# Performance work log

Measured on AMD Instinct MI355X. Metric: run time of the kernel, lower is better.

## Reference

```python
import jax, jax.numpy as jnp
import numpy as np

B, L, D = 2, 2048, 2048
H, KV, HD = 16, 8, 128
EPS = 1e-5
ROPE_BASE = 10000.0
SCALING_ALPHA = 1.0
SCALE = HD ** -0.5


def setup_inputs() -> dict:
    key = jax.random.key(0)
    ks = jax.random.split(key, 5)
    s = 0.02  # weight init scale
    return {
        "x": jax.random.normal(ks[0], (B, L, D), jnp.float32),
        "wq": jax.random.normal(ks[1], (D, H * HD), jnp.float32) * s,
        "wk": jax.random.normal(ks[2], (D, KV * HD), jnp.float32) * s,
        "wv": jax.random.normal(ks[3], (D, KV * HD), jnp.float32) * s,
        "wo": jax.random.normal(ks[4], (H * HD, D), jnp.float32) * s,
        "qn_w": jnp.ones((HD,), jnp.float32),
        "kn_w": jnp.ones((HD,), jnp.float32),
    }


def _rope(t):
    # t: [B, h, L, HD]. DynamicNTKAlpha base scaling (alpha=1 -> no-op).
    base = ROPE_BASE * SCALING_ALPHA ** (HD / (HD - 2))
    # NOTE: source uses base**(+i/d) (no negative exponent) -- kept faithful.
    freqs = base ** (jnp.arange(0, HD, 2, dtype=jnp.float32) / HD)  # [HD/2]
    pos = jnp.arange(t.shape[-2], dtype=jnp.float32)                # [L]
    angles = pos[:, None] * freqs[None, :]                          # [L, HD/2]
    cos, sin = jnp.cos(angles), jnp.sin(angles)
    x1, x2 = t[..., : HD // 2], t[..., HD // 2 :]
    return jnp.concatenate([x1 * cos - x2 * sin, x2 * cos + x1 * sin], axis=-1)


def _rmsnorm(t, w):
    return t * jax.lax.rsqrt(jnp.mean(t * t, axis=-1, keepdims=True) + EPS) * w


def reference(x, wq, wk, wv, wo, qn_w, kn_w):
    b, l, _ = x.shape
    q = (x @ wq).reshape(b, l, H, HD).transpose(0, 2, 1, 3)   # [B,H,L,HD]
    k = (x @ wk).reshape(b, l, KV, HD).transpose(0, 2, 1, 3)  # [B,KV,L,HD]
    v = (x @ wv).reshape(b, l, KV, HD).transpose(0, 2, 1, 3)
    q = _rmsnorm(_rope(q), qn_w)
    k = _rmsnorm(_rope(k), kn_w)
    # GQA: expand KV heads to match query heads
    rep = H // KV
    k = jnp.repeat(k, rep, axis=1)  # [B,H,L,HD]
    v = jnp.repeat(v, rep, axis=1)
    scores = jnp.einsum("bhqd,bhkd->bhqk", q, k) * SCALE
    probs = jax.nn.softmax(scores, axis=-1)
    out = jnp.einsum("bhqk,bhkd->bhqd", probs, v)             # [B,H,L,HD]
    out = out.transpose(0, 2, 1, 3).reshape(b, l, H * HD)
    return out @ wo
```

## Files before the change

kernel.cpp:

```cpp
#include <hip/hip_runtime.h>
#include <math.h>

#define BB 2
#define LL 2048
#define DD 2048
#define HH 16
#define KVH 8
#define HDIM 128
#define SCALE_F 0.08838834764831845f
#define EPS_F 1e-5f
#define LOG2E 1.4426950408889634f
#define SMAX_F 17.0f
#define QKVW 4096

typedef unsigned short u16;
typedef __attribute__((ext_vector_type(8))) short short8;
typedef __attribute__((ext_vector_type(4))) float f32x4;
typedef __attribute__((ext_vector_type(16))) float f32x16;

#define MFMA16(a, b, c) __builtin_amdgcn_mfma_f32_16x16x32_bf16((a), (b), (c), 0, 0, 0)
#define MFMA32(a, b, c) __builtin_amdgcn_mfma_f32_32x32x16_bf16((a), (b), (c), 0, 0, 0)

__device__ __forceinline__ float b2f(u16 u) {
    union { unsigned int i; float f; } x;
    x.i = ((unsigned int)u) << 16;
    return x.f;
}
__device__ __forceinline__ u16 f2b(float f) {
    unsigned int x = __float_as_uint(f);
    unsigned int r = x + 0x7FFFu + ((x >> 16) & 1u);
    return (u16)(r >> 16);
}
__device__ __forceinline__ u16 f2b_fast(float f) {
    return (u16)((__float_as_uint(f) + 0x8000u) >> 16);
}
__device__ __forceinline__ void g2l(const u16* g, u16* l) {
    __builtin_amdgcn_global_load_lds(
        (const __attribute__((address_space(1))) unsigned int*)g,
        (__attribute__((address_space(3))) unsigned int*)l, 16, 0, 0);
}

__global__ __launch_bounds__(256) void convert_f32_bf16(const float* __restrict__ in,
                                                        u16* __restrict__ out, int n) {
    int i = (blockIdx.x * 256 + threadIdx.x) * 4;
    if (i >= n) return;
    float4 v = *(const float4*)(in + i);
    unsigned int p0 = (unsigned int)f2b(v.x) | ((unsigned int)f2b(v.y) << 16);
    unsigned int p1 = (unsigned int)f2b(v.z) | ((unsigned int)f2b(v.w) << 16);
    uint2 pk; pk.x = p0; pk.y = p1;
    *(uint2*)(out + i) = pk;
}

__global__ __launch_bounds__(256) void transpose_conv(const float* __restrict__ in,
                                                      u16* __restrict__ out, int R, int C) {
    __shared__ u16 t[64 * 65];
    int c0 = blockIdx.x * 64, r0 = blockIdx.y * 64;
#pragma unroll
    for (int i = 0; i < 16; i++) {
        int idx = threadIdx.x + i * 256;
        int r = idx >> 6, c = idx & 63;
        t[r * 65 + c] = f2b(in[(size_t)(r0 + r) * C + c0 + c]);
    }
    __syncthreads();
#pragma unroll
    for (int i = 0; i < 16; i++) {
        int idx = threadIdx.x + i * 256;
        int r = idx >> 6, c = idx & 63;
        out[(size_t)(c0 + r) * R + r0 + c] = t[c * 65 + r];
    }
}

__global__ __launch_bounds__(256) void transpose_v(const u16* __restrict__ qkv,
                                                   u16* __restrict__ vt) {
    __shared__ u16 t[64 * 65];
    int l0 = blockIdx.x * 64, d0 = blockIdx.y * 64;
    int bg = blockIdx.z, b = bg >> 3, g = bg & 7;
    const u16* src = qkv + (size_t)b * LL * QKVW + 3072 + g * HDIM;
    u16* dst = vt + (size_t)bg * HDIM * LL;
#pragma unroll
    for (int i = 0; i < 16; i++) {
        int idx = threadIdx.x + i * 256;
        int r = idx >> 6, c = idx & 63;
        t[r * 65 + c] = src[(size_t)(l0 + r) * QKVW + d0 + c];
    }
    __syncthreads();
#pragma unroll
    for (int i = 0; i < 16; i++) {
        int idx = threadIdx.x + i * 256;
        int r = idx >> 6, c = idx & 63;
        dst[(size_t)(d0 + r) * LL + l0 + c] = t[c * 65 + r];
    }
}

__global__ __launch_bounds__(256) void rope_table(float* __restrict__ ct, float* __restrict__ st) {
    int i = blockIdx.x * 256 + threadIdx.x;
    int pos = i >> 6, d = i & 63;
    float freq = (float)pow(10000.0, (double)d * (1.0 / 64.0));
    float ang = (float)pos * freq;
    double a = (double)ang;
    ct[i] = (float)cos(a);
    st[i] = (float)sin(a);
}

template <bool F32OUT>
__global__ __launch_bounds__(256) void gemm_bt(const u16* __restrict__ A,
                                               const u16* __restrict__ Bt,
                                               void* __restrict__ Cv, int M, int N, int K) {
    __shared__ __align__(16) u16 As[128 * 32];
    __shared__ __align__(16) u16 Bs[128 * 32];
    const int tid = threadIdx.x;
    const int w = tid >> 6, lane = tid & 63;
    const int lm = lane & 15, lq = lane >> 4;
    const int bn0 = blockIdx.x * 128, bm0 = blockIdx.y * 128;
    const int wm = (w >> 1) * 64, wn = (w & 1) * 64;

    f32x4 acc[4][4];
#pragma unroll
    for (int i = 0; i < 4; i++)
#pragma unroll
        for (int j = 0; j < 4; j++) acc[i][j] = (f32x4){0.f, 0.f, 0.f, 0.f};

    const int sr = w * 32 + (lane >> 2);
    const int scc = lane & 3;
    const u16* ga = A + (size_t)(bm0 + sr) * K + scc * 8;
    const u16* gb = Bt + (size_t)(bn0 + sr) * K + scc * 8;
    u16* lA = &As[w * 1024];
    u16* lB = &Bs[w * 1024];

    for (int k0 = 0; k0 < K; k0 += 32) {
        __syncthreads();
        g2l(ga + k0, lA);
        g2l(ga + (size_t)16 * K + k0, lA + 512);
        g2l(gb + k0, lB);
        g2l(gb + (size_t)16 * K + k0, lB + 512);
        __syncthreads();

        short8 af[4], bf[4];
#pragma unroll
        for (int mt = 0; mt < 4; mt++)
            af[mt] = *(const short8*)(&As[(wm + mt * 16 + lm) * 32 + lq * 8]);
#pragma unroll
        for (int nt = 0; nt < 4; nt++)
            bf[nt] = *(const short8*)(&Bs[(wn + nt * 16 + lm) * 32 + lq * 8]);
#pragma unroll
        for (int mt = 0; mt < 4; mt++)
#pragma unroll
            for (int nt = 0; nt < 4; nt++) acc[mt][nt] = MFMA16(af[mt], bf[nt], acc[mt][nt]);
    }

#pragma unroll
    for (int mt = 0; mt < 4; mt++)
#pragma unroll
        for (int nt = 0; nt < 4; nt++)
#pragma unroll
            for (int r = 0; r < 4; r++) {
                int row = bm0 + wm + mt * 16 + lq * 4 + r;
                int col = bn0 + wn + nt * 16 + lm;
                if (F32OUT)
                    ((float*)Cv)[(size_t)row * N + col] = acc[mt][nt][r];
                else
                    ((u16*)Cv)[(size_t)row * N + col] = f2b(acc[mt][nt][r]);
            }
}

__global__ __launch_bounds__(256) void rope_norm(u16* __restrict__ qkv,
                                                 const float* __restrict__ qw,
                                                 const float* __restrict__ kw,
                                                 const float* __restrict__ ct,
                                                 const float* __restrict__ st) {
    int slot = blockIdx.x * 4 + (threadIdx.x >> 6);
    int lane = threadIdx.x & 63;
    int hh = slot % (HH + KVH);
    int row = slot / (HH + KVH);
    int pos = row & (LL - 1);

    u16* base = qkv + (size_t)row * QKVW + hh * HDIM;
    const float* w = (hh < HH) ? qw : kw;

    float x1 = b2f(base[lane]), x2 = b2f(base[lane + 64]);
    float c = ct[pos * 64 + lane], s = st[pos * 64 + lane];
    float r1 = x1 * c - x2 * s;
    float r2 = x2 * c + x1 * s;
    float ss = r1 * r1 + r2 * r2;
#pragma unroll
    for (int m = 1; m < 64; m <<= 1) ss += __shfl_xor(ss, m, 64);
    float sc = 1.0f / sqrtf(ss * (1.0f / 128.0f) + EPS_F);
    base[lane] = f2b(r1 * sc * w[lane]);
    base[lane + 64] = f2b(r2 * sc * w[lane + 64]);
}

__global__ __launch_bounds__(256, 2) void attn_kernel(const u16* __restrict__ qkv,
                                                      const u16* __restrict__ vt,
                                                      u16* __restrict__ ob) {
    __shared__ __align__(16) u16 Kt[64 * 128];
    __shared__ __align__(16) u16 Vt[128 * 64];
    __shared__ __align__(16) u16 Ps[4][32 * 64];

    const int tid = threadIdx.x, w = tid >> 6, lane = tid & 63;
    const int l31 = lane & 31, lh = lane >> 5;
    const int q0 = blockIdx.x * 128;
    const int bh = blockIdx.y, b = bh >> 4, hd = bh & 15, g = hd >> 1;

    const u16* kbase = qkv + (size_t)b * LL * QKVW + 2048 + g * HDIM;
    const u16* vtbase = vt + (size_t)(b * KVH + g) * HDIM * LL;

    const int krl = lane >> 4, kgl = lane & 15;
    const int vrl = lane >> 3, vgl = lane & 7;

    const int qrow = q0 + w * 32 + l31;
    short8 aq[8];
    {
        const u16* qp = qkv + (size_t)(b * LL + qrow) * QKVW + hd * HDIM + lh * 8;
#pragma unroll
        for (int kk = 0; kk < 8; kk++) aq[kk] = *(const short8*)(qp + kk * 16);
    }

    f32x16 o[4];
#pragma unroll
    for (int i = 0; i < 4; i++)
#pragma unroll
        for (int r = 0; r < 16; r++) o[i][r] = 0.f;
    float psum[16];
#pragma unroll
    for (int r = 0; r < 16; r++) psum[r] = 0.f;
    const float SC2 = SCALE_F * LOG2E;

    for (int t = 0; t < LL / 64; t++) {
        __syncthreads();
#pragma unroll
        for (int ch = 0; ch < 4; ch++) {
            int r = w * 16 + ch * 4 + krl;
            int gc = kgl ^ (r & 15);
            g2l(kbase + (size_t)(t * 64 + r) * QKVW + gc * 8,
                &Kt[(w * 16 + ch * 4) * 128]);
        }
#pragma unroll
        for (int ch = 0; ch < 4; ch++) {
            int r = w * 32 + ch * 8 + vrl;
            int gc = vgl ^ (r & 7);
            g2l(vtbase + (size_t)r * LL + t * 64 + gc * 8,
                &Vt[(w * 32 + ch * 8) * 64]);
        }
        __syncthreads();

        f32x16 s[2];
#pragma unroll
        for (int kt = 0; kt < 2; kt++) {
#pragma unroll
            for (int r = 0; r < 16; r++) s[kt][r] = 0.f;
            int key = kt * 32 + l31;
#pragma unroll
            for (int kk = 0; kk < 8; kk++) {
                int gg = (kk * 2 + lh) ^ (key & 15);
                short8 bf = *(const short8*)(&Kt[key * 128 + gg * 8]);
                s[kt] = MFMA32(aq[kk], bf, s[kt]);
            }
        }

#pragma unroll
        for (int kt = 0; kt < 2; kt++) {
            int key = kt * 32 + l31;
#pragma unroll
            for (int r = 0; r < 16; r++) {
                float p = exp2f(fmaf(s[kt][r], SC2, -SMAX_F));
                psum[r] += p;
                int row = (r & 3) + 8 * (r >> 2) + 4 * lh;
                Ps[w][row * 64 + (key ^ ((row & 7) << 3))] = f2b_fast(p);
            }
        }
        __syncthreads();

#pragma unroll
        for (int kc = 0; kc < 4; kc++) {
            int gp = ((kc * 2 + lh) ^ (l31 & 7)) * 8;
            short8 pa = *(const short8*)(&Ps[w][l31 * 64 + gp]);
#pragma unroll
            for (int dn = 0; dn < 4; dn++) {
                int d = dn * 32 + l31;
                int gv = ((kc * 2 + lh) ^ (d & 7)) * 8;
                short8 bv = *(const short8*)(&Vt[d * 64 + gv]);
                o[dn] = MFMA32(pa, bv, o[dn]);
            }
        }
    }

#pragma unroll
    for (int m = 1; m < 32; m <<= 1)
#pragma unroll
        for (int r = 0; r < 16; r++) psum[r] += __shfl_xor(psum[r], m, 32);
    float inv[16];
#pragma unroll
    for (int r = 0; r < 16; r++) inv[r] = 1.0f / psum[r];

    u16* obase = ob + (size_t)(b * LL + q0 + w * 32) * (HH * HDIM) + hd * HDIM;
#pragma unroll
    for (int dn = 0; dn < 4; dn++)
#pragma unroll
        for (int r = 0; r < 16; r++) {
            int row = (r & 3) + 8 * (r >> 2) + 4 * lh;
            obase[(size_t)row * (HH * HDIM) + dn * 32 + l31] = f2b(o[dn][r] * inv[r]);
        }
}

extern "C" void kernel_launch(void* const* d_in, const int* in_sizes, int n_in,
                              void* d_out, int out_size, void* d_ws, size_t ws_size,
                              hipStream_t stream) {
    const float* x  = (const float*)d_in[0];
    const float* wq = (const float*)d_in[1];
    const float* wk = (const float*)d_in[2];
    const float* wv = (const float*)d_in[3];
    const float* wo = (const float*)d_in[4];
    const float* qn = (const float*)d_in[5];
    const float* kn = (const float*)d_in[6];

    u16* ws = (u16*)d_ws;
    const size_t SZ_X = (size_t)BB * LL * DD;
    u16* xb    = ws;
    u16* qkv   = xb + SZ_X;
    u16* wqkvT = qkv + (size_t)BB * LL * QKVW;
    u16* woT   = wqkvT + (size_t)QKVW * DD;
    float* ct  = (float*)(woT + (size_t)DD * DD);
    float* st  = ct + (size_t)LL * 64;
    u16* att = xb;
    u16* vt  = wqkvT;

    convert_f32_bf16<<<dim3((unsigned)(SZ_X / 1024)), dim3(256), 0, stream>>>(x, xb, (int)SZ_X);
    transpose_conv<<<dim3(32, 32), dim3(256), 0, stream>>>(wq, wqkvT, DD, DD);
    transpose_conv<<<dim3(16, 32), dim3(256), 0, stream>>>(wk, wqkvT + (size_t)2048 * DD, DD, KVH * HDIM);
    transpose_conv<<<dim3(16, 32), dim3(256), 0, stream>>>(wv, wqkvT + (size_t)3072 * DD, DD, KVH * HDIM);
    transpose_conv<<<dim3(32, 32), dim3(256), 0, stream>>>(wo, woT, HH * HDIM, DD);
    rope_table<<<dim3(LL * 64 / 256), dim3(256), 0, stream>>>(ct, st);

    gemm_bt<false><<<dim3(QKVW / 128, BB * LL / 128), dim3(256), 0, stream>>>(xb, wqkvT, qkv, BB * LL, QKVW, DD);

    rope_norm<<<dim3(BB * LL * (HH + KVH) / 4), dim3(256), 0, stream>>>(qkv, qn, kn, ct, st);
    transpose_v<<<dim3(LL / 64, HDIM / 64, BB * KVH), dim3(256), 0, stream>>>(qkv, vt);

    attn_kernel<<<dim3(LL / 128, BB * HH), dim3(256), 0, stream>>>(qkv, vt, att);
    gemm_bt<true><<<dim3(DD / 128, BB * LL / 128), dim3(256), 0, stream>>>(att, woT, d_out, BB * LL, DD, DD);
}
```

Measured before the change: 412.2 us.

## Merge prep and rope/V-transpose launches and split-K the output projection

The input conversion, the four weight transposes and the rope table build now run in one kernel that dispatches work by block-index range. Rope+RMSNorm and the V transpose are likewise combined into one launch, which cuts launch count and inter-kernel gaps. The output projection GEMM is split along K into two halves that accumulate into a zeroed fp32 output with atomicAdd, doubling the block count for better CU fill. The trade-off is an extra memset plus atomic write traffic on the output, and fp32 summation order that is no longer fixed.

```diff
diff --git a/kernel.cpp b/kernel.cpp
--- a/kernel.cpp
+++ b/kernel.cpp
@@ -40,72 +40,60 @@
         (__attribute__((address_space(3))) unsigned int*)l, 16, 0, 0);
 }
 
-__global__ __launch_bounds__(256) void convert_f32_bf16(const float* __restrict__ in,
-                                                        u16* __restrict__ out, int n) {
-    int i = (blockIdx.x * 256 + threadIdx.x) * 4;
-    if (i >= n) return;
-    float4 v = *(const float4*)(in + i);
-    unsigned int p0 = (unsigned int)f2b(v.x) | ((unsigned int)f2b(v.y) << 16);
-    unsigned int p1 = (unsigned int)f2b(v.z) | ((unsigned int)f2b(v.w) << 16);
-    uint2 pk; pk.x = p0; pk.y = p1;
-    *(uint2*)(out + i) = pk;
-}
-
-__global__ __launch_bounds__(256) void transpose_conv(const float* __restrict__ in,
-                                                      u16* __restrict__ out, int R, int C) {
+__global__ __launch_bounds__(256) void prep_kernel(const float* __restrict__ x,
+                                                   u16* __restrict__ xb,
+                                                   const float* __restrict__ wq,
+                                                   const float* __restrict__ wk,
+                                                   const float* __restrict__ wv,
+                                                   const float* __restrict__ wo,
+                                                   u16* __restrict__ wqkvT,
+                                                   u16* __restrict__ woT,
+                                                   float* __restrict__ ct,
+                                                   float* __restrict__ st) {
     __shared__ u16 t[64 * 65];
-    int c0 = blockIdx.x * 64, r0 = blockIdx.y * 64;
-#pragma unroll
-    for (int i = 0; i < 16; i++) {
-        int idx = threadIdx.x + i * 256;
-        int r = idx >> 6, c = idx & 63;
-        t[r * 65 + c] = f2b(in[(size_t)(r0 + r) * C + c0 + c]);
-    }
-    __syncthreads();
-#pragma unroll
-    for (int i = 0; i < 16; i++) {
-        int idx = threadIdx.x + i * 256;
-        int r = idx >> 6, c = idx & 63;
-        out[(size_t)(c0 + r) * R + r0 + c] = t[c * 65 + r];
-    }
-}
-
-__global__ __launch_bounds__(256) void transpose_v(const u16* __restrict__ qkv,
-                                                   u16* __restrict__ vt) {
-    __shared__ u16 t[64 * 65];
-    int l0 = blockIdx.x * 64, d0 = blockIdx.y * 64;
-    int bg = blockIdx.z, b = bg >> 3, g = bg & 7;
-    const u16* src = qkv + (size_t)b * LL * QKVW + 3072 + g * HDIM;
-    u16* dst = vt + (size_t)bg * HDIM * LL;
-#pragma unroll
-    for (int i = 0; i < 16; i++) {
-        int idx = threadIdx.x + i * 256;
-        int r = idx >> 6, c = idx & 63;
-        t[r * 65 + c] = src[(size_t)(l0 + r) * QKVW + d0 + c];
-    }
-    __syncthreads();
-#pragma unroll
-    for (int i = 0; i < 16; i++) {
-        int idx = threadIdx.x + i * 256;
-        int r = idx >> 6, c = idx & 63;
-        dst[(size_t)(d0 + r) * LL + l0 + c] = t[c * 65 + r];
-    }
-}
-
-__global__ __launch_bounds__(256) void rope_table(float* __restrict__ ct, float* __restrict__ st) {
-    int i = blockIdx.x * 256 + threadIdx.x;
-    int pos = i >> 6, d = i & 63;
-    float freq = (float)pow(10000.0, (double)d * (1.0 / 64.0));
-    float ang = (float)pos * freq;
-    double a = (double)ang;
-    ct[i] = (float)cos(a);
-    st[i] = (float)sin(a);
-}
-
-template <bool F32OUT>
+    const int blk = blockIdx.x, tid = threadIdx.x;
+    if (blk < 8192) {
+        int i = (blk * 256 + tid) * 4;
+        float4 v = *(const float4*)(x + i);
+        unsigned int p0 = (unsigned int)f2b(v.x) | ((unsigned int)f2b(v.y) << 16);
+        unsigned int p1 = (unsigned int)f2b(v.z) | ((unsigned int)f2b(v.w) << 16);
+        uint2 pk; pk.x = p0; pk.y = p1;
+        *(uint2*)(xb + i) = pk;
+    } else if (blk < 11264) {
+        int j = blk - 8192;
+        const float* in; u16* out; int C, bx, by;
+        if (j < 1024)      { in = wq; out = wqkvT;                      C = 2048; bx = j & 31; by = j >> 5; }
+        else if (j < 1536) { j -= 1024; in = wk; out = wqkvT + (size_t)2048 * DD; C = 1024; bx = j & 15; by = j >> 4; }
+        else if (j < 2048) { j -= 1536; in = wv; out = wqkvT + (size_t)3072 * DD; C = 1024; bx = j & 15; by = j >> 4; }
+        else               { j -= 2048; in = wo; out = woT;                      C = 2048; bx = j & 31; by = j >> 5; }
+        int c0 = bx * 64, r0 = by * 64;
+#pragma unroll
+        for (int i = 0; i < 16; i++) {
+            int idx = tid + i * 256;
+            int r = idx >> 6, c = idx & 63;
+            t[r * 65 + c] = f2b(in[(size_t)(r0 + r) * C + c0 + c]);
+        }
+        __syncthreads();
+#pragma unroll
+        for (int i = 0; i < 16; i++) {
+            int idx = tid + i * 256;
+            int r = idx >> 6, c = idx & 63;
+            out[(size_t)(c0 + r) * DD + r0 + c] = t[c * 65 + r];
+        }
+    } else {
+        int i = (blk - 11264) * 256 + tid;
+        int pos = i >> 6, d = i & 63;
+        float freq = (float)pow(10000.0, (double)d * (1.0 / 64.0));
+        float ang = (float)pos * freq;
+        double a = (double)ang;
+        ct[i] = (float)cos(a);
+        st[i] = (float)sin(a);
+    }
+}
+
 __global__ __launch_bounds__(256) void gemm_bt(const u16* __restrict__ A,
                                                const u16* __restrict__ Bt,
-                                               void* __restrict__ Cv, int M, int N, int K) {
+                                               u16* __restrict__ C, int M, int N, int K) {
     __shared__ __align__(16) u16 As[128 * 32];
     __shared__ __align__(16) u16 Bs[128 * 32];
     const int tid = threadIdx.x;
@@ -156,37 +144,117 @@
             for (int r = 0; r < 4; r++) {
                 int row = bm0 + wm + mt * 16 + lq * 4 + r;
                 int col = bn0 + wn + nt * 16 + lm;
-                if (F32OUT)
-                    ((float*)Cv)[(size_t)row * N + col] = acc[mt][nt][r];
-                else
-                    ((u16*)Cv)[(size_t)row * N + col] = f2b(acc[mt][nt][r]);
+                C[(size_t)row * N + col] = f2b(acc[mt][nt][r]);
             }
 }
 
-__global__ __launch_bounds__(256) void rope_norm(u16* __restrict__ qkv,
-                                                 const float* __restrict__ qw,
-                                                 const float* __restrict__ kw,
-                                                 const float* __restrict__ ct,
-                                                 const float* __restrict__ st) {
-    int slot = blockIdx.x * 4 + (threadIdx.x >> 6);
-    int lane = threadIdx.x & 63;
-    int hh = slot % (HH + KVH);
-    int row = slot / (HH + KVH);
-    int pos = row & (LL - 1);
-
-    u16* base = qkv + (size_t)row * QKVW + hh * HDIM;
-    const float* w = (hh < HH) ? qw : kw;
-
-    float x1 = b2f(base[lane]), x2 = b2f(base[lane + 64]);
-    float c = ct[pos * 64 + lane], s = st[pos * 64 + lane];
-    float r1 = x1 * c - x2 * s;
-    float r2 = x2 * c + x1 * s;
-    float ss = r1 * r1 + r2 * r2;
-#pragma unroll
-    for (int m = 1; m < 64; m <<= 1) ss += __shfl_xor(ss, m, 64);
-    float sc = 1.0f / sqrtf(ss * (1.0f / 128.0f) + EPS_F);
-    base[lane] = f2b(r1 * sc * w[lane]);
-    base[lane + 64] = f2b(r2 * sc * w[lane + 64]);
+__global__ __launch_bounds__(256) void gemm_bt_sk(const u16* __restrict__ A,
+                                                  const u16* __restrict__ Bt,
+                                                  float* __restrict__ C, int M, int N, int K) {
+    __shared__ __align__(16) u16 As[128 * 32];
+    __shared__ __align__(16) u16 Bs[128 * 32];
+    const int tid = threadIdx.x;
+    const int w = tid >> 6, lane = tid & 63;
+    const int lm = lane & 15, lq = lane >> 4;
+    const int bn0 = blockIdx.x * 128, bm0 = blockIdx.y * 128;
+    const int wm = (w >> 1) * 64, wn = (w & 1) * 64;
+    const int kbeg = blockIdx.z * (K >> 1), kend = kbeg + (K >> 1);
+
+    f32x4 acc[4][4];
+#pragma unroll
+    for (int i = 0; i < 4; i++)
+#pragma unroll
+        for (int j = 0; j < 4; j++) acc[i][j] = (f32x4){0.f, 0.f, 0.f, 0.f};
+
+    const int sr = w * 32 + (lane >> 2);
+    const int scc = lane & 3;
+    const u16* ga = A + (size_t)(bm0 + sr) * K + scc * 8;
+    const u16* gb = Bt + (size_t)(bn0 + sr) * K + scc * 8;
+    u16* lA = &As[w * 1024];
+    u16* lB = &Bs[w * 1024];
+
+    for (int k0 = kbeg; k0 < kend; k0 += 32) {
+        __syncthreads();
+        g2l(ga + k0, lA);
+        g2l(ga + (size_t)16 * K + k0, lA + 512);
+        g2l(gb + k0, lB);
+        g2l(gb + (size_t)16 * K + k0, lB + 512);
+        __syncthreads();
+
+        short8 af[4], bf[4];
+#pragma unroll
+        for (int mt = 0; mt < 4; mt++)
+            af[mt] = *(const short8*)(&As[(wm + mt * 16 + lm) * 32 + lq * 8]);
+#pragma unroll
+        for (int nt = 0; nt < 4; nt++)
+            bf[nt] = *(const short8*)(&Bs[(wn + nt * 16 + lm) * 32 + lq * 8]);
+#pragma unroll
+        for (int mt = 0; mt < 4; mt++)
+#pragma unroll
+            for (int nt = 0; nt < 4; nt++) acc[mt][nt] = MFMA16(af[mt], bf[nt], acc[mt][nt]);
+    }
+
+#pragma unroll
+    for (int mt = 0; mt < 4; mt++)
+#pragma unroll
+        for (int nt = 0; nt < 4; nt++)
+#pragma unroll
+            for (int r = 0; r < 4; r++) {
+                int row = bm0 + wm + mt * 16 + lq * 4 + r;
+                int col = bn0 + wn + nt * 16 + lm;
+                atomicAdd(&C[(size_t)row * N + col], acc[mt][nt][r]);
+            }
+}
+
+__global__ __launch_bounds__(256) void ropetv_kernel(u16* __restrict__ qkv,
+                                                     u16* __restrict__ vt,
+                                                     const float* __restrict__ qw,
+                                                     const float* __restrict__ kw,
+                                                     const float* __restrict__ ct,
+                                                     const float* __restrict__ st) {
+    __shared__ u16 t[64 * 65];
+    const int blk = blockIdx.x, tid = threadIdx.x;
+    if (blk < 24576) {
+        int slot = blk * 4 + (tid >> 6);
+        int lane = tid & 63;
+        int hh = slot % (HH + KVH);
+        int row = slot / (HH + KVH);
+        int pos = row & (LL - 1);
+
+        u16* base = qkv + (size_t)row * QKVW + hh * HDIM;
+        const float* w = (hh < HH) ? qw : kw;
+
+        float x1 = b2f(base[lane]), x2 = b2f(base[lane + 64]);
+        float c = ct[pos * 64 + lane], s = st[pos * 64 + lane];
+        float r1 = x1 * c - x2 * s;
+        float r2 = x2 * c + x1 * s;
+        float ss = r1 * r1 + r2 * r2;
+#pragma unroll
+        for (int m = 1; m < 64; m <<= 1) ss += __shfl_xor(ss, m, 64);
+        float sc = 1.0f / sqrtf(ss * (1.0f / 128.0f) + EPS_F);
+        base[lane] = f2b(r1 * sc * w[lane]);
+        base[lane + 64] = f2b(r2 * sc * w[lane + 64]);
+    } else {
+        int j = blk - 24576;
+        int bx = j & 31, by = (j >> 5) & 1, bg = j >> 6;
+        int l0 = bx * 64, d0 = by * 64;
+        int b = bg >> 3, g = bg & 7;
+        const u16* src = qkv + (size_t)b * LL * QKVW + 3072 + g * HDIM;
+        u16* dst = vt + (size_t)bg * HDIM * LL;
+#pragma unroll
+        for (int i = 0; i < 16; i++) {
+            int idx = tid + i * 256;
+            int r = idx >> 6, c = idx & 63;
+            t[r * 65 + c] = src[(size_t)(l0 + r) * QKVW + d0 + c];
+        }
+        __syncthreads();
+#pragma unroll
+        for (int i = 0; i < 16; i++) {
+            int idx = tid + i * 256;
+            int r = idx >> 6, c = idx & 63;
+            dst[(size_t)(d0 + r) * LL + l0 + c] = t[c * 65 + r];
+        }
+    }
 }
 
 __global__ __launch_bounds__(256, 2) void attn_kernel(const u16* __restrict__ qkv,
@@ -324,18 +392,11 @@
     u16* att = xb;
     u16* vt  = wqkvT;
 
-    convert_f32_bf16<<<dim3((unsigned)(SZ_X / 1024)), dim3(256), 0, stream>>>(x, xb, (int)SZ_X);
-    transpose_conv<<<dim3(32, 32), dim3(256), 0, stream>>>(wq, wqkvT, DD, DD);
-    transpose_conv<<<dim3(16, 32), dim3(256), 0, stream>>>(wk, wqkvT + (size_t)2048 * DD, DD, KVH * HDIM);
-    transpose_conv<<<dim3(16, 32), dim3(256), 0, stream>>>(wv, wqkvT + (size_t)3072 * DD, DD, KVH * HDIM);
-    transpose_conv<<<dim3(32, 32), dim3(256), 0, stream>>>(wo, woT, HH * HDIM, DD);
-    rope_table<<<dim3(LL * 64 / 256), dim3(256), 0, stream>>>(ct, st);
-
-    gemm_bt<false><<<dim3(QKVW / 128, BB * LL / 128), dim3(256), 0, stream>>>(xb, wqkvT, qkv, BB * LL, QKVW, DD);
-
-    rope_norm<<<dim3(BB * LL * (HH + KVH) / 4), dim3(256), 0, stream>>>(qkv, qn, kn, ct, st);
-    transpose_v<<<dim3(LL / 64, HDIM / 64, BB * KVH), dim3(256), 0, stream>>>(qkv, vt);
-
+    prep_kernel<<<dim3(11776), dim3(256), 0, stream>>>(x, xb, wq, wk, wv, wo,
+                                                       wqkvT, woT, ct, st);
+    gemm_bt<<<dim3(QKVW / 128, BB * LL / 128), dim3(256), 0, stream>>>(xb, wqkvT, qkv, BB * LL, QKVW, DD);
+    ropetv_kernel<<<dim3(25600), dim3(256), 0, stream>>>(qkv, vt, qn, kn, ct, st);
     attn_kernel<<<dim3(LL / 128, BB * HH), dim3(256), 0, stream>>>(qkv, vt, att);
-    gemm_bt<true><<<dim3(DD / 128, BB * LL / 128), dim3(256), 0, stream>>>(att, woT, d_out, BB * LL, DD, DD);
-}
+    hipMemsetAsync(d_out, 0, (size_t)out_size * sizeof(float), stream);
+    gemm_bt_sk<<<dim3(DD / 128, BB * LL / 128, 2), dim3(256), 0, stream>>>(att, woT, (float*)d_out, BB * LL, DD, DD);
+}
```

Measured after the change: 439.0 us. 6.5% more time.
